# Optimization experiments

Hardware: AMD Instinct MI355X
Metric: run time of the kernel (lower is better)

Reference implementation:

```python
import jax, jax.numpy as jnp
import numpy as np

MASK_RADIUS = 30.0

def _fft_mask(height, width, mode):
    # replicates fft_filter_def: grid over full H rows and rfft half-plane cols
    cht, cwt = height // 2, width // 2
    fy, fx = jnp.meshgrid(jnp.arange(height), jnp.arange(width // 2 + 1), indexing='ij')
    dist = jnp.sqrt((fx - cwt).astype(jnp.float32) ** 2 + (fy - cht).astype(jnp.float32) ** 2)
    if mode == 'high':
        return (dist > MASK_RADIUS).astype(jnp.float32)
    return (dist <= MASK_RADIUS).astype(jnp.float32)


def setup_inputs() -> dict:
    key = jax.random.key(0)
    k1, k2, k3 = jax.random.split(key, 3)
    B, Cin, Cout, H, W, K = 4, 64, 64, 128, 128, 3
    x = jax.random.normal(k1, (B, Cin, H, W), dtype=jnp.float32)
    weight = jax.random.normal(k2, (Cout, Cin, K, K), dtype=jnp.float32) * 0.1
    bias = jax.random.normal(k3, (Cout,), dtype=jnp.float32) * 0.1
    return {"x": x, "weight": weight, "bias": bias}


def reference(x, weight, bias):
    B, Cin, H, W = x.shape
    x = x.astype(jnp.float32)
    # rfft2 of input, then fftshift (as in original; kernel FFT is NOT shifted)
    fft_x = jnp.fft.rfft2(x)                          # [B, Cin, H, W//2+1]
    fft_x = jnp.fft.fftshift(fft_x, axes=(-2, -1))
    kernel_fft = jnp.fft.rfft2(weight, s=(H, W))      # [Cout, Cin, H, W//2+1]
    # high-pass frequency mask (fft_filter == 'high')
    mask = _fft_mask(H, W, 'high')                    # [H, W//2+1]
    fft_x = fft_x * mask
    # per-frequency complex GEMV over in_channels (avoids [B,Cout,Cin,H,Wf] blowup)
    fft_out = jnp.einsum('bihw,oihw->bohw', fft_x, kernel_fft)
    out = jnp.fft.irfft2(fft_out, s=(H, W))           # [B, Cout, H, W]
    return out + bias[None, :, None, None]
```

## Files before the change

### kernel.cpp

```cpp
#include <hip/hip_runtime.h>

#define PI_F 3.14159265358979323846f

#define HH 128
#define WW 128
#define WF 65
#define NB 4
#define NC 64
#define CPLX_PER_IMG (HH * WF)

typedef __attribute__((ext_vector_type(8))) short short8;
typedef __attribute__((ext_vector_type(4))) float f32x4;

__device__ __forceinline__ ushort f2b(float f) {
    unsigned u = __float_as_uint(f);
    u += 0x7fffu + ((u >> 16) & 1u);
    return (ushort)(u >> 16);
}


__device__ __forceinline__ void pre_item_tail(int idx, const float* __restrict__ w,
                                              ushort* __restrict__ A4,
                                              ushort* __restrict__ A5,
                                              ushort* __restrict__ WvRe,
                                              ushort* __restrict__ WvIm) {
    if (idx < 151552) {
        int j = idx - 86016;
        int m = j >> 8, k2 = j & 255;
        int part = m >> 7, h = m & 127;
        int kp = k2 >> 7, u = k2 & 127;
        float s, c;
        __sincosf(2.f * PI_F * (float)((u * h) & 127) / 128.f, &s, &c);
        float val = part == 0 ? (kp == 0 ? c : -s) : (kp == 0 ? s : c);
        A4[j] = f2b(val * (1.f / 128.f));
    } else if (idx < 172032) {
        int j = idx - 151552;
        int x = j / 160, k2 = j - x * 160;
        int part = k2 / 80, v = k2 - part * 80;
        float s, c;
        __sincosf(2.f * PI_F * (float)((v * x) & 127) / 128.f, &s, &c);
        float cv = (v == 0 || v == 64) ? 1.f : 2.f;
        float val = (v < 65) ? (part == 0 ? cv * c : -cv * s) * (1.f / 128.f) : 0.f;
        A5[j] = f2b(val);
    } else {
        int xw = idx - 172032;
        int i = xw & 63;
        int o = (xw >> 6) & 63;
        int pv = xw >> 12;
        int p = pv / WF;
        int v = pv % WF;
        const float* wp = w + ((size_t)o * 64 + i) * 9 + p * 3;
        float re = wp[0], im = 0.f;
#pragma unroll
        for (int q = 1; q <= 2; ++q) {
            int k = (v * q) & 127;
            float s, c;
            __sincosf(-2.f * PI_F * (float)k / 128.f, &s, &c);
            re += wp[q] * c;
            im += wp[q] * s;
        }
        WvRe[xw] = f2b(re);
        WvIm[xw] = f2b(im);
    }
}

#define B2P 280
#define A1P 136
__global__ __launch_bounds__(1024) void k_fwd(const float* __restrict__ x,
                                              const float* __restrict__ w,
                                              ushort* __restrict__ XsRe,
                                              ushort* __restrict__ XsIm,
                                              ushort* __restrict__ WvRe,
                                              ushort* __restrict__ WvIm,
                                              ushort* __restrict__ A4,
                                              ushort* __restrict__ A5) {
    __shared__ ushort A1L[160 * A1P];
    __shared__ ushort B2[80 * B2P];
    __shared__ __align__(16) float2 TW[128];
    int t = threadIdx.x;
    int img = blockIdx.x;
    const float* gx = x + (size_t)img * 16384;

    if (t < 128) {
        float s, c;
        __sincosf(2.f * PI_F * (float)t / 128.f, &s, &c);
        TW[t] = make_float2(c, s);
    }
    for (int idx = t; idx < 20480; idx += 1024) {
        int m = idx >> 7, k = idx & 127;
        int part = m / 80, v = m - part * 80;
        float s, c;
        __sincosf(2.f * PI_F * (float)((v * k) & 127) / 128.f, &s, &c);
        float val = (v < 65) ? (part ? -s : c) : 0.f;
        A1L[m * A1P + k] = f2b(val);
    }
    {
        int gtid = img * 1024 + t;
        for (int idx = 86016 + gtid; idx < 970752; idx += 262144)
            pre_item_tail(idx, w, A4, A5, WvRe, WvIm);
    }
    __syncthreads();

    int lane = t & 63, wave = t >> 6;
    int lrow = lane & 15, lq = lane >> 4;

    {
        int g = wave >> 3, nt = wave & 7;
        int hrow = nt * 16 + lrow;
        f32x4 acc[5];
#pragma unroll
        for (int j = 0; j < 5; ++j) acc[j] = (f32x4){0.f, 0.f, 0.f, 0.f};
#pragma unroll
        for (int ks = 0; ks < 4; ++ks) {
            const float* xp = gx + hrow * 128 + ks * 32 + lq * 8;
            float4 f0 = *(const float4*)xp;
            float4 f1 = *(const float4*)(xp + 4);
            short8 b;
            b[0] = (short)f2b(f0.x); b[1] = (short)f2b(f0.y);
            b[2] = (short)f2b(f0.z); b[3] = (short)f2b(f0.w);
            b[4] = (short)f2b(f1.x); b[5] = (short)f2b(f1.y);
            b[6] = (short)f2b(f1.z); b[7] = (short)f2b(f1.w);
#pragma unroll
            for (int j = 0; j < 5; ++j) {
                int mt = g * 5 + j;
                short8 a = *(const short8*)&A1L[(mt * 16 + lrow) * A1P + ks * 32 + lq * 8];
                acc[j] = __builtin_amdgcn_mfma_f32_16x16x32_bf16(a, b, acc[j], 0, 0, 0);
            }
        }
#pragma unroll
        for (int j = 0; j < 5; ++j) {
            int m0 = (g * 5 + j) * 16 + lq * 4;
            int part = m0 >= 80;
            int v0 = m0 - part * 80;
#pragma unroll
            for (int e = 0; e < 4; ++e)
                B2[(v0 + e) * B2P + part * 128 + hrow] = f2b(acc[j][e]);
        }
    }
    __syncthreads();

    {
        int nt = wave;
        int part = nt >= 8;
        int um = (nt & 7) * 16 + lrow;
        f32x4 acc[5];
#pragma unroll
        for (int mt = 0; mt < 5; ++mt) acc[mt] = (f32x4){0.f, 0.f, 0.f, 0.f};
#pragma unroll
        for (int ks = 0; ks < 8; ++ks) {
            int kp = ks >> 2;
            int hbase = (ks & 3) * 32 + lq * 8;
            short8 bfr;
            int idx = (um * hbase) & 127;
#pragma unroll
            for (int e = 0; e < 8; ++e) {
                float2 tw = TW[idx];
                float val = !part ? (kp == 0 ? tw.x : tw.y)
                                  : (kp == 0 ? -tw.y : tw.x);
                bfr[e] = (short)f2b(val);
                idx = (idx + um) & 127;
            }
#pragma unroll
            for (int mt = 0; mt < 5; ++mt) {
                short8 a = *(short8*)&B2[(mt * 16 + lrow) * B2P + ks * 32 + lq * 8];
                acc[mt] = __builtin_amdgcn_mfma_f32_16x16x32_bf16(a, bfr, acc[mt], 0, 0, 0);
            }
        }
        int u = (nt & 7) * 16 + lrow;
        int u_out = (u + 64) & 127;
        int du = u_out - 64;
        ushort* dimg = (part ? XsIm : XsRe) + (size_t)img * CPLX_PER_IMG;
#pragma unroll
        for (int mt = 0; mt < 5; ++mt)
#pragma unroll
            for (int e = 0; e < 4; ++e) {
                int v_in = mt * 16 + lq * 4 + e;
                if (v_in < 65) {
                    int v_out = v_in + 32; if (v_out >= 65) v_out -= 65;
                    int dv = v_out - 64;
                    bool keep = (du * du + dv * dv) > 900;
                    dimg[v_out * 128 + u_out] = keep ? f2b(acc[mt][e]) : (ushort)0;
                }
            }
    }
}

#define AP 72
__global__ __launch_bounds__(256, 2) void k_gemm(const ushort* __restrict__ XsRe,
                                                 const ushort* __restrict__ XsIm,
                                                 const ushort* __restrict__ WvRe,
                                                 const ushort* __restrict__ WvIm,
                                                 ushort* __restrict__ Zre,
                                                 ushort* __restrict__ Zim) {
    __shared__ ushort XTre[128 * AP], XTim[128 * AP];
    __shared__ ushort WSre[64 * AP],  WSim[64 * AP];
    int t = threadIdx.x;
    int v = blockIdx.x >> 2;
    int b = blockIdx.x & 3;
    {
        int u = t & 127, qh = t >> 7;
#pragma unroll
        for (int q8 = 0; q8 < 8; ++q8) {
            int q = qh * 8 + q8;
            ushort re4[4], im4[4];
#pragma unroll
            for (int c = 0; c < 4; ++c) {
                int i = q * 4 + c;
                size_t off = ((size_t)(b * 64 + i) * WF + v) * 128 + u;
                re4[c] = XsRe[off];
                im4[c] = XsIm[off];
            }
            *(ushort4*)&XTre[u * AP + q * 4] = make_ushort4(re4[0], re4[1], re4[2], re4[3]);
            *(ushort4*)&XTim[u * AP + q * 4] = make_ushort4(im4[0], im4[1], im4[2], im4[3]);
        }
    }
    int lane = t & 63, wave = t >> 6;
    int lrow = lane & 15, lq = lane >> 4;
    int u0 = wave * 32;
    f32x4 fRe[8], fIm[8];
#pragma unroll
    for (int m = 0; m < 8; ++m) {
        fRe[m] = (f32x4){0.f, 0.f, 0.f, 0.f};
        fIm[m] = (f32x4){0.f, 0.f, 0.f, 0.f};
    }
    for (int p = 0; p < 3; ++p) {
        if (p) __syncthreads();
        {
            const ushort* gr = WvRe + ((size_t)(p * WF + v)) * 4096;
            const ushort* gi = WvIm + ((size_t)(p * WF + v)) * 4096;
#pragma unroll
            for (int cc = 0; cc < 2; ++cc) {
                int c = t + cc * 256;
                int o = c >> 3, i0 = (c & 7) * 8;
                *(short8*)&WSre[o * AP + i0] = *(const short8*)&gr[c * 8];
                *(short8*)&WSim[o * AP + i0] = *(const short8*)&gi[c * 8];
            }
        }
        __syncthreads();
        f32x4 pRe[8], pIm[8];
#pragma unroll
        for (int m = 0; m < 8; ++m) {
            pRe[m] = (f32x4){0.f, 0.f, 0.f, 0.f};
            pIm[m] = (f32x4){0.f, 0.f, 0.f, 0.f};
        }
#pragma unroll
        for (int ks = 0; ks < 2; ++ks) {
            int kb = ks * 32 + lq * 8;
            short8 br[2], bi[2], bin[2];
#pragma unroll
            for (int ut = 0; ut < 2; ++ut) {
                int u = u0 + ut * 16 + lrow;
                br[ut] = *(const short8*)&XTre[u * AP + kb];
                bi[ut] = *(const short8*)&XTim[u * AP + kb];
                bin[ut] = bi[ut] ^ (short)0x8000;
            }
#pragma unroll
            for (int ot = 0; ot < 4; ++ot) {
                int o = ot * 16 + lrow;
                short8 ar = *(const short8*)&WSre[o * AP + kb];
                short8 ai = *(const short8*)&WSim[o * AP + kb];
#pragma unroll
                for (int ut = 0; ut < 2; ++ut) {
                    int m = ot * 2 + ut;
                    pRe[m] = __builtin_amdgcn_mfma_f32_16x16x32_bf16(ai, bin[ut], pRe[m], 0, 0, 0);
                    pRe[m] = __builtin_amdgcn_mfma_f32_16x16x32_bf16(ar, br[ut],  pRe[m], 0, 0, 0);
                    pIm[m] = __builtin_amdgcn_mfma_f32_16x16x32_bf16(ai, br[ut],  pIm[m], 0, 0, 0);
                    pIm[m] = __builtin_amdgcn_mfma_f32_16x16x32_bf16(ar, bi[ut],  pIm[m], 0, 0, 0);
                }
            }
        }
#pragma unroll
        for (int ut = 0; ut < 2; ++ut) {
            int u = u0 + ut * 16 + lrow;
            float sn, cn;
            __sincosf(-2.f * PI_F * (float)(u * p) / 128.f, &sn, &cn);
#pragma unroll
            for (int ot = 0; ot < 4; ++ot) {
                int m = ot * 2 + ut;
#pragma unroll
                for (int e = 0; e < 4; ++e) {
                    fRe[m][e] += pRe[m][e] * cn - pIm[m][e] * sn;
                    fIm[m][e] += pIm[m][e] * cn + pRe[m][e] * sn;
                }
            }
        }
    }
#pragma unroll
    for (int ot = 0; ot < 4; ++ot)
#pragma unroll
        for (int ut = 0; ut < 2; ++ut) {
            int m = ot * 2 + ut;
            int u = u0 + ut * 16 + lrow;
#pragma unroll
            for (int e = 0; e < 4; ++e) {
                int o = ot * 16 + lq * 4 + e;
                size_t idx = ((size_t)(b * 64 + o) * WF + v) * 128 + u;
                Zre[idx] = f2b(fRe[m][e]);
                Zim[idx] = f2b(fIm[m][e]);
            }
        }
}

#define B3P 168
__global__ __launch_bounds__(1024) void k_inv(const ushort* __restrict__ Zre,
                                              const ushort* __restrict__ Zim,
                                              const ushort* __restrict__ A4,
                                              const ushort* __restrict__ A5,
                                              const float* __restrict__ bias,
                                              float* __restrict__ out) {
    __shared__ ushort B1[80 * B2P];
    __shared__ ushort B2[128 * B3P];
    int t = threadIdx.x;
    int ch = blockIdx.x;
    for (int c = t; c < 2080; c += 1024) {
        int r = c >> 5, sl = c & 31;
        const ushort* src = (sl < 16 ? Zre : Zim) + ((size_t)ch * WF + r) * 128 + (sl & 15) * 8;
        *(short8*)&B1[r * B2P + sl * 8] = *(const short8*)src;
    }
    if (t < 480) {
        int r = 65 + (t >> 5), sl = t & 31;
        short8 z = {0, 0, 0, 0, 0, 0, 0, 0};
        *(short8*)&B1[r * B2P + sl * 8] = z;
    }
    __syncthreads();
    int lane = t & 63, wave = t >> 6;
    int lrow = lane & 15, lq = lane >> 4;

    {
        int mt = wave;
        f32x4 acc[5];
#pragma unroll
        for (int nt = 0; nt < 5; ++nt) acc[nt] = (f32x4){0.f, 0.f, 0.f, 0.f};
#pragma unroll
        for (int ks = 0; ks < 8; ++ks) {
            short8 a = *(const short8*)&A4[(mt * 16 + lrow) * 256 + ks * 32 + lq * 8];
#pragma unroll
            for (int nt = 0; nt < 5; ++nt) {
                short8 b = *(short8*)&B1[(nt * 16 + lrow) * B2P + ks * 32 + lq * 8];
                acc[nt] = __builtin_amdgcn_mfma_f32_16x16x32_bf16(a, b, acc[nt], 0, 0, 0);
            }
        }
        int part = mt >= 8;
        int h0 = mt * 16 + lq * 4 - part * 128;
#pragma unroll
        for (int nt = 0; nt < 5; ++nt) {
            int v = nt * 16 + lrow;
#pragma unroll
            for (int e = 0; e < 4; ++e)
                B2[(h0 + e) * B3P + part * 80 + v] = f2b(acc[nt][e]);
        }
    }
    __syncthreads();

    {
        int mt = wave & 7, nh = wave >> 3;
        f32x4 acc[4];
#pragma unroll
        for (int jn = 0; jn < 4; ++jn) acc[jn] = (f32x4){0.f, 0.f, 0.f, 0.f};
#pragma unroll
        for (int ks = 0; ks < 5; ++ks) {
            short8 a = *(short8*)&B2[(mt * 16 + lrow) * B3P + ks * 32 + lq * 8];
#pragma unroll
            for (int jn = 0; jn < 4; ++jn) {
                int nt = nh * 4 + jn;
                short8 b = *(const short8*)&A5[(nt * 16 + lrow) * 160 + ks * 32 + lq * 8];
                acc[jn] = __builtin_amdgcn_mfma_f32_16x16x32_bf16(a, b, acc[jn], 0, 0, 0);
            }
        }
        float bo = bias[ch & 63];
        float* go = out + (size_t)ch * 16384;
#pragma unroll
        for (int jn = 0; jn < 4; ++jn) {
            int xx = (nh * 4 + jn) * 16 + lrow;
#pragma unroll
            for (int e = 0; e < 4; ++e) {
                int h = mt * 16 + lq * 4 + e;
                go[h * 128 + xx] = acc[jn][e] + bo;
            }
        }
    }
}

extern "C" void kernel_launch(void* const* d_in, const int* in_sizes, int n_in,
                              void* d_out, int out_size, void* d_ws, size_t ws_size,
                              hipStream_t stream) {
    const float* x = (const float*)d_in[0];
    const float* w = (const float*)d_in[1];
    const float* bias = (const float*)d_in[2];
    float* out = (float*)d_out;

    char* ws = (char*)d_ws;
    ushort* A4   = (ushort*)(ws + 172032);
    ushort* A5   = (ushort*)(ws + 303104);
    ushort* WvRe = (ushort*)(ws + 344064);
    ushort* WvIm = (ushort*)(ws + 1941504);
    ushort* XsRe = (ushort*)(ws + 12058624);
    ushort* XsIm = (ushort*)(ws + 16318464);
    ushort* Zre  = (ushort*)(ws + 20578304);
    ushort* Zim  = (ushort*)(ws + 24838144);

    k_fwd<<<NB * NC, 1024, 0, stream>>>(x, w, XsRe, XsIm, WvRe, WvIm, A4, A5);
    k_gemm<<<WF * NB, 256, 0, stream>>>(XsRe, XsIm, WvRe, WvIm, Zre, Zim);
    k_inv<<<NB * NC, 1024, 0, stream>>>(Zre, Zim, A4, A5, bias, out);
}
```

Before: 46.92 us.

## Fuse frequency GEMM and inverse FFT into one kernel with grid barrier

Merges the per-frequency channel-mixing GEMM and the inverse-transform kernel into a single 256-block, 1024-thread kernel. An atomic-counter grid barrier, reset by the forward kernel, separates the two phases, which removes one kernel launch and its drain and fill gap. The GEMM phase is retiled so each wave handles one output-channel tile, and 4 leftover tiles are looped over by a few blocks. The spin barrier assumes all 256 blocks are co-resident. The uneven 260-tile split makes a few blocks do twice the GEMM work before everyone waits.

After: 130.8 us. 179% more time.

```diff
diff --git a/kernel.cpp b/kernel.cpp
--- a/kernel.cpp
+++ b/kernel.cpp
@@ -73,13 +73,16 @@
                                               ushort* __restrict__ WvRe,
                                               ushort* __restrict__ WvIm,
                                               ushort* __restrict__ A4,
-                                              ushort* __restrict__ A5) {
+                                              ushort* __restrict__ A5,
+                                              unsigned int* __restrict__ ctr) {
     __shared__ ushort A1L[160 * A1P];
     __shared__ ushort B2[80 * B2P];
     __shared__ __align__(16) float2 TW[128];
     int t = threadIdx.x;
     int img = blockIdx.x;
     const float* gx = x + (size_t)img * 16384;
+
+    if (img == 0 && t == 0) *ctr = 0;
 
     if (t < 128) {
         float s, c;
@@ -185,197 +188,199 @@
     }
 }
 
-#define AP 72
-__global__ __launch_bounds__(256, 2) void k_gemm(const ushort* __restrict__ XsRe,
-                                                 const ushort* __restrict__ XsIm,
-                                                 const ushort* __restrict__ WvRe,
-                                                 const ushort* __restrict__ WvIm,
-                                                 ushort* __restrict__ Zre,
-                                                 ushort* __restrict__ Zim) {
-    __shared__ ushort XTre[128 * AP], XTim[128 * AP];
-    __shared__ ushort WSre[64 * AP],  WSim[64 * AP];
+#define AP  72
+#define B3P 168
+__global__ __launch_bounds__(1024) void k_mi(const ushort* __restrict__ XsRe,
+                                             const ushort* __restrict__ XsIm,
+                                             const ushort* __restrict__ WvRe,
+                                             const ushort* __restrict__ WvIm,
+                                             ushort* __restrict__ Zre,
+                                             ushort* __restrict__ Zim,
+                                             const ushort* __restrict__ A4,
+                                             const ushort* __restrict__ A5,
+                                             const float* __restrict__ bias,
+                                             float* __restrict__ out,
+                                             unsigned int* __restrict__ ctr) {
+    __shared__ __align__(16) ushort POOL[43904];
     int t = threadIdx.x;
-    int v = blockIdx.x >> 2;
-    int b = blockIdx.x & 3;
-    {
-        int u = t & 127, qh = t >> 7;
-#pragma unroll
-        for (int q8 = 0; q8 < 8; ++q8) {
-            int q = qh * 8 + q8;
-            ushort re4[4], im4[4];
-#pragma unroll
-            for (int c = 0; c < 4; ++c) {
-                int i = q * 4 + c;
-                size_t off = ((size_t)(b * 64 + i) * WF + v) * 128 + u;
-                re4[c] = XsRe[off];
-                im4[c] = XsIm[off];
-            }
-            *(ushort4*)&XTre[u * AP + q * 4] = make_ushort4(re4[0], re4[1], re4[2], re4[3]);
-            *(ushort4*)&XTim[u * AP + q * 4] = make_ushort4(im4[0], im4[1], im4[2], im4[3]);
-        }
-    }
+    int bid = blockIdx.x;
     int lane = t & 63, wave = t >> 6;
     int lrow = lane & 15, lq = lane >> 4;
-    int u0 = wave * 32;
-    f32x4 fRe[8], fIm[8];
-#pragma unroll
-    for (int m = 0; m < 8; ++m) {
-        fRe[m] = (f32x4){0.f, 0.f, 0.f, 0.f};
-        fIm[m] = (f32x4){0.f, 0.f, 0.f, 0.f};
-    }
-    for (int p = 0; p < 3; ++p) {
-        if (p) __syncthreads();
-        {
-            const ushort* gr = WvRe + ((size_t)(p * WF + v)) * 4096;
-            const ushort* gi = WvIm + ((size_t)(p * WF + v)) * 4096;
-#pragma unroll
-            for (int cc = 0; cc < 2; ++cc) {
-                int c = t + cc * 256;
-                int o = c >> 3, i0 = (c & 7) * 8;
-                *(short8*)&WSre[o * AP + i0] = *(const short8*)&gr[c * 8];
-                *(short8*)&WSim[o * AP + i0] = *(const short8*)&gi[c * 8];
-            }
-        }
-        __syncthreads();
-        f32x4 pRe[8], pIm[8];
-#pragma unroll
-        for (int m = 0; m < 8; ++m) {
-            pRe[m] = (f32x4){0.f, 0.f, 0.f, 0.f};
-            pIm[m] = (f32x4){0.f, 0.f, 0.f, 0.f};
-        }
-#pragma unroll
-        for (int ks = 0; ks < 2; ++ks) {
-            int kb = ks * 32 + lq * 8;
-            short8 br[2], bi[2], bin[2];
+
+    {
+        ushort* XTre = POOL;
+        ushort* XTim = POOL + 128 * AP;
+        ushort* WSre = POOL + 2 * 128 * AP;
+        ushort* WSim = POOL + 2 * 128 * AP + 64 * AP;
+        for (int tile = bid; tile < 260; tile += 256) {
+            int v = tile >> 2, b = tile & 3;
+            __syncthreads();
+            {
+                int u = t & 127, q = t >> 7;
+                const ushort* bR = XsRe + ((size_t)(b * 64 + q * 8) * WF + v) * 128 + u;
+                const ushort* bI = XsIm + ((size_t)(b * 64 + q * 8) * WF + v) * 128 + u;
+                short8 vr, vi;
+#pragma unroll
+                for (int c = 0; c < 8; ++c) {
+                    vr[c] = (short)bR[(size_t)c * WF * 128];
+                    vi[c] = (short)bI[(size_t)c * WF * 128];
+                }
+                *(short8*)&XTre[u * AP + q * 8] = vr;
+                *(short8*)&XTim[u * AP + q * 8] = vi;
+            }
+            int uq = wave >> 2, ot = wave & 3;
+            int u0 = uq * 32;
+            f32x4 fRe[2], fIm[2];
+#pragma unroll
+            for (int m = 0; m < 2; ++m) {
+                fRe[m] = (f32x4){0.f, 0.f, 0.f, 0.f};
+                fIm[m] = (f32x4){0.f, 0.f, 0.f, 0.f};
+            }
+            for (int p = 0; p < 3; ++p) {
+                __syncthreads();
+                {
+                    const ushort* gr = WvRe + ((size_t)(p * WF + v)) * 4096;
+                    const ushort* gi = WvIm + ((size_t)(p * WF + v)) * 4096;
+                    if (t < 512) {
+                        int o = t >> 3, i0 = (t & 7) * 8;
+                        *(short8*)&WSre[o * AP + i0] = *(const short8*)&gr[t * 8];
+                    } else {
+                        int c = t - 512;
+                        int o = c >> 3, i0 = (c & 7) * 8;
+                        *(short8*)&WSim[o * AP + i0] = *(const short8*)&gi[c * 8];
+                    }
+                }
+                __syncthreads();
+                f32x4 pRe[2], pIm[2];
+#pragma unroll
+                for (int m = 0; m < 2; ++m) {
+                    pRe[m] = (f32x4){0.f, 0.f, 0.f, 0.f};
+                    pIm[m] = (f32x4){0.f, 0.f, 0.f, 0.f};
+                }
+#pragma unroll
+                for (int ks = 0; ks < 2; ++ks) {
+                    int kb = ks * 32 + lq * 8;
+                    short8 br[2], bi[2], bin[2];
+#pragma unroll
+                    for (int ut = 0; ut < 2; ++ut) {
+                        int u = u0 + ut * 16 + lrow;
+                        br[ut] = *(const short8*)&XTre[u * AP + kb];
+                        bi[ut] = *(const short8*)&XTim[u * AP + kb];
+                        bin[ut] = bi[ut] ^ (short)0x8000;
+                    }
+                    int o = ot * 16 + lrow;
+                    short8 ar = *(const short8*)&WSre[o * AP + kb];
+                    short8 ai = *(const short8*)&WSim[o * AP + kb];
+#pragma unroll
+                    for (int ut = 0; ut < 2; ++ut) {
+                        pRe[ut] = __builtin_amdgcn_mfma_f32_16x16x32_bf16(ai, bin[ut], pRe[ut], 0, 0, 0);
+                        pRe[ut] = __builtin_amdgcn_mfma_f32_16x16x32_bf16(ar, br[ut],  pRe[ut], 0, 0, 0);
+                        pIm[ut] = __builtin_amdgcn_mfma_f32_16x16x32_bf16(ai, br[ut],  pIm[ut], 0, 0, 0);
+                        pIm[ut] = __builtin_amdgcn_mfma_f32_16x16x32_bf16(ar, bi[ut],  pIm[ut], 0, 0, 0);
+                    }
+                }
+#pragma unroll
+                for (int ut = 0; ut < 2; ++ut) {
+                    int u = u0 + ut * 16 + lrow;
+                    float sn, cn;
+                    __sincosf(-2.f * PI_F * (float)((u * p) & 127) / 128.f, &sn, &cn);
+#pragma unroll
+                    for (int e = 0; e < 4; ++e) {
+                        fRe[ut][e] += pRe[ut][e] * cn - pIm[ut][e] * sn;
+                        fIm[ut][e] += pIm[ut][e] * cn + pRe[ut][e] * sn;
+                    }
+                }
+            }
 #pragma unroll
             for (int ut = 0; ut < 2; ++ut) {
                 int u = u0 + ut * 16 + lrow;
-                br[ut] = *(const short8*)&XTre[u * AP + kb];
-                bi[ut] = *(const short8*)&XTim[u * AP + kb];
-                bin[ut] = bi[ut] ^ (short)0x8000;
-            }
-#pragma unroll
-            for (int ot = 0; ot < 4; ++ot) {
-                int o = ot * 16 + lrow;
-                short8 ar = *(const short8*)&WSre[o * AP + kb];
-                short8 ai = *(const short8*)&WSim[o * AP + kb];
-#pragma unroll
-                for (int ut = 0; ut < 2; ++ut) {
-                    int m = ot * 2 + ut;
-                    pRe[m] = __builtin_amdgcn_mfma_f32_16x16x32_bf16(ai, bin[ut], pRe[m], 0, 0, 0);
-                    pRe[m] = __builtin_amdgcn_mfma_f32_16x16x32_bf16(ar, br[ut],  pRe[m], 0, 0, 0);
-                    pIm[m] = __builtin_amdgcn_mfma_f32_16x16x32_bf16(ai, br[ut],  pIm[m], 0, 0, 0);
-                    pIm[m] = __builtin_amdgcn_mfma_f32_16x16x32_bf16(ar, bi[ut],  pIm[m], 0, 0, 0);
-                }
-            }
-        }
-#pragma unroll
-        for (int ut = 0; ut < 2; ++ut) {
-            int u = u0 + ut * 16 + lrow;
-            float sn, cn;
-            __sincosf(-2.f * PI_F * (float)(u * p) / 128.f, &sn, &cn);
-#pragma unroll
-            for (int ot = 0; ot < 4; ++ot) {
-                int m = ot * 2 + ut;
 #pragma unroll
                 for (int e = 0; e < 4; ++e) {
-                    fRe[m][e] += pRe[m][e] * cn - pIm[m][e] * sn;
-                    fIm[m][e] += pIm[m][e] * cn + pRe[m][e] * sn;
-                }
-            }
-        }
-    }
-#pragma unroll
-    for (int ot = 0; ot < 4; ++ot)
-#pragma unroll
-        for (int ut = 0; ut < 2; ++ut) {
-            int m = ot * 2 + ut;
-            int u = u0 + ut * 16 + lrow;
-#pragma unroll
-            for (int e = 0; e < 4; ++e) {
-                int o = ot * 16 + lq * 4 + e;
-                size_t idx = ((size_t)(b * 64 + o) * WF + v) * 128 + u;
-                Zre[idx] = f2b(fRe[m][e]);
-                Zim[idx] = f2b(fIm[m][e]);
-            }
-        }
-}
-
-#define B3P 168
-__global__ __launch_bounds__(1024) void k_inv(const ushort* __restrict__ Zre,
-                                              const ushort* __restrict__ Zim,
-                                              const ushort* __restrict__ A4,
-                                              const ushort* __restrict__ A5,
-                                              const float* __restrict__ bias,
-                                              float* __restrict__ out) {
-    __shared__ ushort B1[80 * B2P];
-    __shared__ ushort B2[128 * B3P];
-    int t = threadIdx.x;
-    int ch = blockIdx.x;
-    for (int c = t; c < 2080; c += 1024) {
-        int r = c >> 5, sl = c & 31;
-        const ushort* src = (sl < 16 ? Zre : Zim) + ((size_t)ch * WF + r) * 128 + (sl & 15) * 8;
-        *(short8*)&B1[r * B2P + sl * 8] = *(const short8*)src;
-    }
-    if (t < 480) {
-        int r = 65 + (t >> 5), sl = t & 31;
-        short8 z = {0, 0, 0, 0, 0, 0, 0, 0};
-        *(short8*)&B1[r * B2P + sl * 8] = z;
-    }
+                    int o = ot * 16 + lq * 4 + e;
+                    size_t idx = ((size_t)(b * 64 + o) * WF + v) * 128 + u;
+                    Zre[idx] = f2b(fRe[ut][e]);
+                    Zim[idx] = f2b(fIm[ut][e]);
+                }
+            }
+        }
+    }
+
     __syncthreads();
-    int lane = t & 63, wave = t >> 6;
-    int lrow = lane & 15, lq = lane >> 4;
+    if (t == 0) {
+        __threadfence();
+        atomicAdd(ctr, 1u);
+        while (atomicAdd(ctr, 0u) < 256u) __builtin_amdgcn_s_sleep(8);
+    }
+    __syncthreads();
+    __threadfence();
 
     {
-        int mt = wave;
-        f32x4 acc[5];
-#pragma unroll
-        for (int nt = 0; nt < 5; ++nt) acc[nt] = (f32x4){0.f, 0.f, 0.f, 0.f};
-#pragma unroll
-        for (int ks = 0; ks < 8; ++ks) {
-            short8 a = *(const short8*)&A4[(mt * 16 + lrow) * 256 + ks * 32 + lq * 8];
+        ushort* B1 = POOL;
+        ushort* B2 = POOL + 80 * B2P;
+        int ch = bid;
+        for (int c = t; c < 2080; c += 1024) {
+            int r = c >> 5, sl = c & 31;
+            const ushort* src = (sl < 16 ? Zre : Zim) + ((size_t)ch * WF + r) * 128 + (sl & 15) * 8;
+            *(short8*)&B1[r * B2P + sl * 8] = *(const short8*)src;
+        }
+        if (t < 480) {
+            int r = 65 + (t >> 5), sl = t & 31;
+            short8 z = {0, 0, 0, 0, 0, 0, 0, 0};
+            *(short8*)&B1[r * B2P + sl * 8] = z;
+        }
+        __syncthreads();
+
+        {
+            int mt = wave;
+            f32x4 acc[5];
+#pragma unroll
+            for (int nt = 0; nt < 5; ++nt) acc[nt] = (f32x4){0.f, 0.f, 0.f, 0.f};
+#pragma unroll
+            for (int ks = 0; ks < 8; ++ks) {
+                short8 a = *(const short8*)&A4[(mt * 16 + lrow) * 256 + ks * 32 + lq * 8];
+#pragma unroll
+                for (int nt = 0; nt < 5; ++nt) {
+                    short8 b = *(short8*)&B1[(nt * 16 + lrow) * B2P + ks * 32 + lq * 8];
+                    acc[nt] = __builtin_amdgcn_mfma_f32_16x16x32_bf16(a, b, acc[nt], 0, 0, 0);
+                }
+            }
+            int part = mt >= 8;
+            int h0 = mt * 16 + lq * 4 - part * 128;
 #pragma unroll
             for (int nt = 0; nt < 5; ++nt) {
-                short8 b = *(short8*)&B1[(nt * 16 + lrow) * B2P + ks * 32 + lq * 8];
-                acc[nt] = __builtin_amdgcn_mfma_f32_16x16x32_bf16(a, b, acc[nt], 0, 0, 0);
-            }
-        }
-        int part = mt >= 8;
-        int h0 = mt * 16 + lq * 4 - part * 128;
-#pragma unroll
-        for (int nt = 0; nt < 5; ++nt) {
-            int v = nt * 16 + lrow;
-#pragma unroll
-            for (int e = 0; e < 4; ++e)
-                B2[(h0 + e) * B3P + part * 80 + v] = f2b(acc[nt][e]);
-        }
-    }
-    __syncthreads();
-
-    {
-        int mt = wave & 7, nh = wave >> 3;
-        f32x4 acc[4];
-#pragma unroll
-        for (int jn = 0; jn < 4; ++jn) acc[jn] = (f32x4){0.f, 0.f, 0.f, 0.f};
-#pragma unroll
-        for (int ks = 0; ks < 5; ++ks) {
-            short8 a = *(short8*)&B2[(mt * 16 + lrow) * B3P + ks * 32 + lq * 8];
+                int v = nt * 16 + lrow;
+#pragma unroll
+                for (int e = 0; e < 4; ++e)
+                    B2[(h0 + e) * B3P + part * 80 + v] = f2b(acc[nt][e]);
+            }
+        }
+        __syncthreads();
+
+        {
+            int mt = wave & 7, nh = wave >> 3;
+            f32x4 acc[4];
+#pragma unroll
+            for (int jn = 0; jn < 4; ++jn) acc[jn] = (f32x4){0.f, 0.f, 0.f, 0.f};
+#pragma unroll
+            for (int ks = 0; ks < 5; ++ks) {
+                short8 a = *(short8*)&B2[(mt * 16 + lrow) * B3P + ks * 32 + lq * 8];
+#pragma unroll
+                for (int jn = 0; jn < 4; ++jn) {
+                    int nt = nh * 4 + jn;
+                    short8 b = *(const short8*)&A5[(nt * 16 + lrow) * 160 + ks * 32 + lq * 8];
+                    acc[jn] = __builtin_amdgcn_mfma_f32_16x16x32_bf16(a, b, acc[jn], 0, 0, 0);
+                }
+            }
+            float bo = bias[ch & 63];
+            float* go = out + (size_t)ch * 16384;
 #pragma unroll
             for (int jn = 0; jn < 4; ++jn) {
-                int nt = nh * 4 + jn;
-                short8 b = *(const short8*)&A5[(nt * 16 + lrow) * 160 + ks * 32 + lq * 8];
-                acc[jn] = __builtin_amdgcn_mfma_f32_16x16x32_bf16(a, b, acc[jn], 0, 0, 0);
-            }
-        }
-        float bo = bias[ch & 63];
-        float* go = out + (size_t)ch * 16384;
-#pragma unroll
-        for (int jn = 0; jn < 4; ++jn) {
-            int xx = (nh * 4 + jn) * 16 + lrow;
-#pragma unroll
-            for (int e = 0; e < 4; ++e) {
-                int h = mt * 16 + lq * 4 + e;
-                go[h * 128 + xx] = acc[jn][e] + bo;
+                int xx = (nh * 4 + jn) * 16 + lrow;
+#pragma unroll
+                for (int e = 0; e < 4; ++e) {
+                    int h = mt * 16 + lq * 4 + e;
+                    go[h * 128 + xx] = acc[jn][e] + bo;
+                }
             }
         }
     }
@@ -390,6 +395,7 @@
     float* out = (float*)d_out;
 
     char* ws = (char*)d_ws;
+    unsigned int* ctr = (unsigned int*)(ws + 0);
     ushort* A4   = (ushort*)(ws + 172032);
     ushort* A5   = (ushort*)(ws + 303104);
     ushort* WvRe = (ushort*)(ws + 344064);
@@ -399,7 +405,6 @@
     ushort* Zre  = (ushort*)(ws + 20578304);
     ushort* Zim  = (ushort*)(ws + 24838144);
 
-    k_fwd<<<NB * NC, 1024, 0, stream>>>(x, w, XsRe, XsIm, WvRe, WvIm, A4, A5);
-    k_gemm<<<WF * NB, 256, 0, stream>>>(XsRe, XsIm, WvRe, WvIm, Zre, Zim);
-    k_inv<<<NB * NC, 1024, 0, stream>>>(Zre, Zim, A4, A5, bias, out);
+    k_fwd<<<NB * NC, 1024, 0, stream>>>(x, w, XsRe, XsIm, WvRe, WvIm, A4, A5, ctr);
+    k_mi<<<256, 1024, 0, stream>>>(XsRe, XsIm, WvRe, WvIm, Zre, Zim, A4, A5, bias, out, ctr);
 }
```

## Hoist input loads before table setup and preload all weight taps in GEMM

Applied to the files above, without the earlier changes.

In the forward FFT kernel, the input rows are loaded and converted to bf16 before the twiddle and DFT-matrix tables are built, so global load latency overlaps with the table setup. In the GEMM kernel, all three weight tap slices are staged into shared memory up front instead of one per loop iteration. This removes the per-iteration barriers and lets the weight loads overlap with the input transpose. The cost is triple the weight shared memory and dropping the min-blocks-per-CU launch hint, which may reduce occupancy.

After: 48.62 us. 1.04x slower.

```diff
diff --git a/kernel.cpp b/kernel.cpp
--- a/kernel.cpp
+++ b/kernel.cpp
@@ -80,6 +80,22 @@
     int t = threadIdx.x;
     int img = blockIdx.x;
     const float* gx = x + (size_t)img * 16384;
+    int lane = t & 63, wave = t >> 6;
+    int lrow = lane & 15, lq = lane >> 4;
+
+    int g = wave >> 3, nt8 = wave & 7;
+    int hrow = nt8 * 16 + lrow;
+    short8 bfr[4];
+#pragma unroll
+    for (int ks = 0; ks < 4; ++ks) {
+        const float* xp = gx + hrow * 128 + ks * 32 + lq * 8;
+        float4 f0 = *(const float4*)xp;
+        float4 f1 = *(const float4*)(xp + 4);
+        bfr[ks][0] = (short)f2b(f0.x); bfr[ks][1] = (short)f2b(f0.y);
+        bfr[ks][2] = (short)f2b(f0.z); bfr[ks][3] = (short)f2b(f0.w);
+        bfr[ks][4] = (short)f2b(f1.x); bfr[ks][5] = (short)f2b(f1.y);
+        bfr[ks][6] = (short)f2b(f1.z); bfr[ks][7] = (short)f2b(f1.w);
+    }
 
     if (t < 128) {
         float s, c;
@@ -101,30 +117,17 @@
     }
     __syncthreads();
 
-    int lane = t & 63, wave = t >> 6;
-    int lrow = lane & 15, lq = lane >> 4;
-
-    {
-        int g = wave >> 3, nt = wave & 7;
-        int hrow = nt * 16 + lrow;
+    {
         f32x4 acc[5];
 #pragma unroll
         for (int j = 0; j < 5; ++j) acc[j] = (f32x4){0.f, 0.f, 0.f, 0.f};
 #pragma unroll
         for (int ks = 0; ks < 4; ++ks) {
-            const float* xp = gx + hrow * 128 + ks * 32 + lq * 8;
-            float4 f0 = *(const float4*)xp;
-            float4 f1 = *(const float4*)(xp + 4);
-            short8 b;
-            b[0] = (short)f2b(f0.x); b[1] = (short)f2b(f0.y);
-            b[2] = (short)f2b(f0.z); b[3] = (short)f2b(f0.w);
-            b[4] = (short)f2b(f1.x); b[5] = (short)f2b(f1.y);
-            b[6] = (short)f2b(f1.z); b[7] = (short)f2b(f1.w);
 #pragma unroll
             for (int j = 0; j < 5; ++j) {
                 int mt = g * 5 + j;
                 short8 a = *(const short8*)&A1L[(mt * 16 + lrow) * A1P + ks * 32 + lq * 8];
-                acc[j] = __builtin_amdgcn_mfma_f32_16x16x32_bf16(a, b, acc[j], 0, 0, 0);
+                acc[j] = __builtin_amdgcn_mfma_f32_16x16x32_bf16(a, bfr[ks], acc[j], 0, 0, 0);
             }
         }
 #pragma unroll
@@ -150,20 +153,20 @@
         for (int ks = 0; ks < 8; ++ks) {
             int kp = ks >> 2;
             int hbase = (ks & 3) * 32 + lq * 8;
-            short8 bfr;
+            short8 bb;
             int idx = (um * hbase) & 127;
 #pragma unroll
             for (int e = 0; e < 8; ++e) {
                 float2 tw = TW[idx];
                 float val = !part ? (kp == 0 ? tw.x : tw.y)
                                   : (kp == 0 ? -tw.y : tw.x);
-                bfr[e] = (short)f2b(val);
+                bb[e] = (short)f2b(val);
                 idx = (idx + um) & 127;
             }
 #pragma unroll
             for (int mt = 0; mt < 5; ++mt) {
                 short8 a = *(short8*)&B2[(mt * 16 + lrow) * B2P + ks * 32 + lq * 8];
-                acc[mt] = __builtin_amdgcn_mfma_f32_16x16x32_bf16(a, bfr, acc[mt], 0, 0, 0);
+                acc[mt] = __builtin_amdgcn_mfma_f32_16x16x32_bf16(a, bb, acc[mt], 0, 0, 0);
             }
         }
         int u = (nt & 7) * 16 + lrow;
@@ -186,14 +189,14 @@
 }
 
 #define AP 72
-__global__ __launch_bounds__(256, 2) void k_gemm(const ushort* __restrict__ XsRe,
-                                                 const ushort* __restrict__ XsIm,
-                                                 const ushort* __restrict__ WvRe,
-                                                 const ushort* __restrict__ WvIm,
-                                                 ushort* __restrict__ Zre,
-                                                 ushort* __restrict__ Zim) {
+__global__ __launch_bounds__(256) void k_gemm(const ushort* __restrict__ XsRe,
+                                              const ushort* __restrict__ XsIm,
+                                              const ushort* __restrict__ WvRe,
+                                              const ushort* __restrict__ WvIm,
+                                              ushort* __restrict__ Zre,
+                                              ushort* __restrict__ Zim) {
     __shared__ ushort XTre[128 * AP], XTim[128 * AP];
-    __shared__ ushort WSre[64 * AP],  WSim[64 * AP];
+    __shared__ ushort WSre[3 * 64 * AP], WSim[3 * 64 * AP];
     int t = threadIdx.x;
     int v = blockIdx.x >> 2;
     int b = blockIdx.x & 3;
@@ -214,6 +217,22 @@
             *(ushort4*)&XTim[u * AP + q * 4] = make_ushort4(im4[0], im4[1], im4[2], im4[3]);
         }
     }
+    {
+#pragma unroll
+        for (int pp = 0; pp < 3; ++pp) {
+            const ushort* gr = WvRe + ((size_t)(pp * WF + v)) * 4096;
+            const ushort* gi = WvIm + ((size_t)(pp * WF + v)) * 4096;
+#pragma unroll
+            for (int cc = 0; cc < 2; ++cc) {
+                int c = t + cc * 256;
+                int o = c >> 3, i0 = (c & 7) * 8;
+                *(short8*)&WSre[pp * 64 * AP + o * AP + i0] = *(const short8*)&gr[c * 8];
+                *(short8*)&WSim[pp * 64 * AP + o * AP + i0] = *(const short8*)&gi[c * 8];
+            }
+        }
+    }
+    __syncthreads();
+
     int lane = t & 63, wave = t >> 6;
     int lrow = lane & 15, lq = lane >> 4;
     int u0 = wave * 32;
@@ -224,19 +243,8 @@
         fIm[m] = (f32x4){0.f, 0.f, 0.f, 0.f};
     }
     for (int p = 0; p < 3; ++p) {
-        if (p) __syncthreads();
-        {
-            const ushort* gr = WvRe + ((size_t)(p * WF + v)) * 4096;
-            const ushort* gi = WvIm + ((size_t)(p * WF + v)) * 4096;
-#pragma unroll
-            for (int cc = 0; cc < 2; ++cc) {
-                int c = t + cc * 256;
-                int o = c >> 3, i0 = (c & 7) * 8;
-                *(short8*)&WSre[o * AP + i0] = *(const short8*)&gr[c * 8];
-                *(short8*)&WSim[o * AP + i0] = *(const short8*)&gi[c * 8];
-            }
-        }
-        __syncthreads();
+        const ushort* wsr = WSre + p * 64 * AP;
+        const ushort* wsi = WSim + p * 64 * AP;
         f32x4 pRe[8], pIm[8];
 #pragma unroll
         for (int m = 0; m < 8; ++m) {
@@ -257,8 +265,8 @@
 #pragma unroll
             for (int ot = 0; ot < 4; ++ot) {
                 int o = ot * 16 + lrow;
-                short8 ar = *(const short8*)&WSre[o * AP + kb];
-                short8 ai = *(const short8*)&WSim[o * AP + kb];
+                short8 ar = *(const short8*)&wsr[o * AP + kb];
+                short8 ai = *(const short8*)&wsi[o * AP + kb];
 #pragma unroll
                 for (int ut = 0; ut < 2; ++ut) {
                     int m = ot * 2 + ut;
```
